# Performance work log

Measured on AMD Instinct MI355X. Metric: run time of the kernel, lower is better.

## Reference

```python
import jax, jax.numpy as jnp
import numpy as np

N_NODES = 100000
N_FEAT = 256
N_EDGES = 3200000
N_CLUSTERS = 16
COLLAPSE_REG = 0.1


def setup_inputs() -> dict:
    key = jax.random.key(0)
    k1, k2, k3, k4 = jax.random.split(key, 4)
    features = jax.random.normal(k1, (N_NODES, N_FEAT), dtype=jnp.float32)
    edge_row = jax.random.randint(k2, (N_EDGES,), 0, N_NODES, dtype=jnp.int32)
    edge_col = jax.random.randint(k3, (N_EDGES,), 0, N_NODES, dtype=jnp.int32)
    edge_val = jnp.ones((N_EDGES,), dtype=jnp.float32)
    # orthogonal-ish init approximated by scaled normal (init does not affect math)
    W = jax.random.normal(k4, (N_FEAT, N_CLUSTERS), dtype=jnp.float32) / np.float32(np.sqrt(N_FEAT))
    b = jnp.zeros((N_CLUSTERS,), dtype=jnp.float32)
    return {"features": features, "W": W, "b": b,
            "edge_row": edge_row, "edge_col": edge_col, "edge_val": edge_val}


def reference(features, W, b, edge_row, edge_col, edge_val):
    n = features.shape[0]
    k = W.shape[1]
    # assignment softmax (dropout_rate=0 -> identity)
    assignments = jax.nn.softmax(features @ W + b, axis=1)  # [n, k]
    cluster_sizes = assignments.sum(axis=0)                  # [k]
    assignments_pooling = assignments / cluster_sizes        # [n, k]
    # degrees = sparse row sums of adjacency
    degrees = jax.ops.segment_sum(edge_val, edge_row, num_segments=n)[:, None]  # [n, 1]
    n_edges = degrees.sum() / 2
    # sparse mm: adjacency @ assignments via gather + segment_sum
    adj_assign = jax.ops.segment_sum(edge_val[:, None] * assignments[edge_col],
                                     edge_row, num_segments=n)  # [n, k]
    graph_pooled = assignments.T @ adj_assign                # [k, k]
    normalizer_left = assignments.T @ degrees                # [k, 1]
    normalizer_right = degrees.T @ assignments               # [1, k]
    normalizer = normalizer_left @ normalizer_right / (2 * n_edges)
    spectral_loss = -jnp.trace(graph_pooled - normalizer) / (2 * n_edges)
    collapse_loss = COLLAPSE_REG * (jnp.linalg.norm(cluster_sizes) / n
                                    * jnp.sqrt(jnp.float32(k)) - 1.0)
    features_pooled = jax.nn.selu(assignments_pooling.T @ features)  # [k, d]
    return features_pooled, assignments, spectral_loss, collapse_loss
```

## Files before the change

### kernel.cpp

```cpp
#include <hip/hip_runtime.h>
#include <math.h>

#define KC 16
#define DF 256

#define WS_POOLED 0
#define WS_CS     4096
#define WS_M      4112
#define WS_TR     4128
#define WS_ESUM   4129
#define WS_TOTAL  4130
#define SHDW_OFF_BYTES 16640


typedef float floatx2 __attribute__((ext_vector_type(2)));

__global__ void zero_ws_kernel(float* __restrict__ ws) {
  int i = blockIdx.x * blockDim.x + threadIdx.x;
  if (i < WS_TOTAL) ws[i] = 0.0f;
}

__device__ __forceinline__ void cvt16_fp8(uint4 u, float* f) {
  floatx2 p;
  p = __builtin_amdgcn_cvt_pk_f32_fp8(u.x, false); f[0] = p[0];  f[1] = p[1];
  p = __builtin_amdgcn_cvt_pk_f32_fp8(u.x, true);  f[2] = p[0];  f[3] = p[1];
  p = __builtin_amdgcn_cvt_pk_f32_fp8(u.y, false); f[4] = p[0];  f[5] = p[1];
  p = __builtin_amdgcn_cvt_pk_f32_fp8(u.y, true);  f[6] = p[0];  f[7] = p[1];
  p = __builtin_amdgcn_cvt_pk_f32_fp8(u.z, false); f[8] = p[0];  f[9] = p[1];
  p = __builtin_amdgcn_cvt_pk_f32_fp8(u.z, true);  f[10] = p[0]; f[11] = p[1];
  p = __builtin_amdgcn_cvt_pk_f32_fp8(u.w, false); f[12] = p[0]; f[13] = p[1];
  p = __builtin_amdgcn_cvt_pk_f32_fp8(u.w, true);  f[14] = p[0]; f[15] = p[1];
}

__global__ void __launch_bounds__(256) assign_kernel(
    const float* __restrict__ F, const float* __restrict__ W,
    const float* __restrict__ b, float* __restrict__ S,
    unsigned* __restrict__ Sh, float* __restrict__ ws, int n) {
  __shared__ float Ft[32 * 257];
  __shared__ float cs_l[KC];
  const int t = threadIdx.x;
  if (t < KC) cs_l[t] = 0.0f;
  const int nb = blockIdx.x << 8;
  const int node = nb + t;
  const bool valid = node < n;
  const bool interior = (nb + 256 <= n);

  const int nl = t >> 3;
  const int jc = t & 7;

  float4 pref[8];
  auto load_chunk = [&](int s) {
    #pragma unroll
    for (int it = 0; it < 8; ++it) {
      const int nn = nl + (it << 5);
      if (interior || nb + nn < n)
        pref[it] = *(const float4*)&F[(size_t)(nb + nn) * DF + (s << 5) + (jc << 2)];
      else
        pref[it] = make_float4(0.f, 0.f, 0.f, 0.f);
    }
  };

  float acc[KC];
  #pragma unroll
  for (int k = 0; k < KC; ++k) acc[k] = 0.f;

  load_chunk(0);
  for (int s = 0; s < 8; ++s) {
    __syncthreads();
    #pragma unroll
    for (int it = 0; it < 8; ++it) {
      const int nn = nl + (it << 5);
      const int d0 = jc << 2;
      Ft[(d0 + 0) * 257 + nn] = pref[it].x;
      Ft[(d0 + 1) * 257 + nn] = pref[it].y;
      Ft[(d0 + 2) * 257 + nn] = pref[it].z;
      Ft[(d0 + 3) * 257 + nn] = pref[it].w;
    }
    __syncthreads();
    if (s < 7) load_chunk(s + 1);
    #pragma unroll
    for (int j = 0; j < 8; ++j) {
      const float fv0 = Ft[(4 * j + 0) * 257 + t];
      const float fv1 = Ft[(4 * j + 1) * 257 + t];
      const float fv2 = Ft[(4 * j + 2) * 257 + t];
      const float fv3 = Ft[(4 * j + 3) * 257 + t];
      const float* __restrict__ Wg = &W[(size_t)((s << 5) + (j << 2)) * KC];
      #pragma unroll
      for (int k = 0; k < KC; ++k)
        acc[k] += fv0 * Wg[k] + fv1 * Wg[KC + k]
                + fv2 * Wg[2 * KC + k] + fv3 * Wg[3 * KC + k];
    }
  }

  float mx = -1e30f;
  #pragma unroll
  for (int k = 0; k < KC; ++k) { acc[k] += b[k]; mx = fmaxf(mx, acc[k]); }
  float sum = 0.f;
  #pragma unroll
  for (int k = 0; k < KC; ++k) { acc[k] = __expf(acc[k] - mx); sum += acc[k]; }
  const float inv = 1.0f / sum;
  #pragma unroll
  for (int k = 0; k < KC; ++k) acc[k] *= inv;
  if (!valid) {
    #pragma unroll
    for (int k = 0; k < KC; ++k) acc[k] = 0.f;
  }
  if (valid) {
    float4* __restrict__ So = (float4*)&S[(size_t)node * KC];
    So[0] = make_float4(acc[0],  acc[1],  acc[2],  acc[3]);
    So[1] = make_float4(acc[4],  acc[5],  acc[6],  acc[7]);
    So[2] = make_float4(acc[8],  acc[9],  acc[10], acc[11]);
    So[3] = make_float4(acc[12], acc[13], acc[14], acc[15]);
    if (Sh) {
      unsigned w0, w1, w2, w3;
      w0 = __builtin_amdgcn_cvt_pk_fp8_f32(acc[0],  acc[1],  0,  false);
      w0 = __builtin_amdgcn_cvt_pk_fp8_f32(acc[2],  acc[3],  w0, true);
      w1 = __builtin_amdgcn_cvt_pk_fp8_f32(acc[4],  acc[5],  0,  false);
      w1 = __builtin_amdgcn_cvt_pk_fp8_f32(acc[6],  acc[7],  w1, true);
      w2 = __builtin_amdgcn_cvt_pk_fp8_f32(acc[8],  acc[9],  0,  false);
      w2 = __builtin_amdgcn_cvt_pk_fp8_f32(acc[10], acc[11], w2, true);
      w3 = __builtin_amdgcn_cvt_pk_fp8_f32(acc[12], acc[13], 0,  false);
      w3 = __builtin_amdgcn_cvt_pk_fp8_f32(acc[14], acc[15], w3, true);
      *(uint4*)&Sh[(size_t)node * 4] = make_uint4(w0, w1, w2, w3);
    }
  }
  #pragma unroll
  for (int off = 1; off < 64; off <<= 1) {
    #pragma unroll
    for (int k = 0; k < KC; ++k) acc[k] += __shfl_xor(acc[k], off);
  }
  if ((t & 63) == 0) {
    #pragma unroll
    for (int k = 0; k < KC; ++k) atomicAdd(&cs_l[k], acc[k]);
  }
  __syncthreads();
  if (t < KC) atomicAdd(&ws[WS_CS + t], cs_l[t]);
}

__global__ void __launch_bounds__(256) edge_kernel_fp8(
    const int* __restrict__ erow, const int* __restrict__ ecol,
    const float* __restrict__ evl, const uint4* __restrict__ S8,
    float* __restrict__ ws, int ne) {
  __shared__ float red[KC + 2];
  const int t = threadIdx.x;
  if (t < KC + 2) red[t] = 0.0f;
  __syncthreads();

  float m[KC];
  #pragma unroll
  for (int i = 0; i < KC; ++i) m[i] = 0.f;
  float tr = 0.f, es = 0.f;

  const int tid = blockIdx.x * 256 + t;
  const int stride = gridDim.x * 256;
  for (int e0 = tid; e0 < ne; e0 += 8 * stride) {
    int r[8], c[8];
    float v[8];
    #pragma unroll
    for (int q = 0; q < 8; ++q) {
      const int e = e0 + q * stride;
      const bool ok = (q == 0) || (e < ne);
      r[q] = ok ? erow[e] : 0;
      c[q] = ok ? ecol[e] : 0;
      v[q] = ok ? evl[e] : 0.f;
    }
    uint4 A[8], B[8];
    #pragma unroll
    for (int q = 0; q < 8; ++q) { A[q] = S8[r[q]]; B[q] = S8[c[q]]; }
    #pragma unroll
    for (int q = 0; q < 8; ++q) {
      float a[16], bb[16];
      cvt16_fp8(A[q], a);
      cvt16_fp8(B[q], bb);
      float d = 0.f;
      #pragma unroll
      for (int k = 0; k < 16; ++k) d += a[k] * bb[k];
      tr += v[q] * d;
      es += v[q];
      #pragma unroll
      for (int k = 0; k < 16; ++k) m[k] += v[q] * a[k];
    }
  }
  #pragma unroll
  for (int off = 1; off < 64; off <<= 1) {
    tr += __shfl_xor(tr, off);
    es += __shfl_xor(es, off);
    #pragma unroll
    for (int i = 0; i < KC; ++i) m[i] += __shfl_xor(m[i], off);
  }
  if ((t & 63) == 0) {
    atomicAdd(&red[KC], tr);
    atomicAdd(&red[KC + 1], es);
    #pragma unroll
    for (int i = 0; i < KC; ++i) atomicAdd(&red[i], m[i]);
  }
  __syncthreads();
  if (t < KC)            atomicAdd(&ws[WS_M + t], red[t]);
  else if (t == KC)      atomicAdd(&ws[WS_TR], red[KC]);
  else if (t == KC + 1)  atomicAdd(&ws[WS_ESUM], red[KC + 1]);
}

__global__ void __launch_bounds__(256) edge_kernel_f32(
    const int* __restrict__ erow, const int* __restrict__ ecol,
    const float* __restrict__ evl, const float* __restrict__ S,
    float* __restrict__ ws, int ne) {
  __shared__ float red[KC + 2];
  const int t = threadIdx.x;
  if (t < KC + 2) red[t] = 0.0f;
  __syncthreads();
  float m[KC];
  #pragma unroll
  for (int i = 0; i < KC; ++i) m[i] = 0.f;
  float tr = 0.f, es = 0.f;
  const int stride = gridDim.x * blockDim.x;
  for (int e = blockIdx.x * blockDim.x + t; e < ne; e += stride) {
    const int r = erow[e];
    const int c = ecol[e];
    const float v = evl[e];
    const float4* __restrict__ Sr = (const float4*)(S + (size_t)r * KC);
    const float4* __restrict__ Sc = (const float4*)(S + (size_t)c * KC);
    const float4 a0 = Sr[0], a1 = Sr[1], a2 = Sr[2], a3 = Sr[3];
    const float4 b0 = Sc[0], b1 = Sc[1], b2 = Sc[2], b3 = Sc[3];
    float d = a0.x*b0.x + a0.y*b0.y + a0.z*b0.z + a0.w*b0.w
            + a1.x*b1.x + a1.y*b1.y + a1.z*b1.z + a1.w*b1.w
            + a2.x*b2.x + a2.y*b2.y + a2.z*b2.z + a2.w*b2.w
            + a3.x*b3.x + a3.y*b3.y + a3.z*b3.z + a3.w*b3.w;
    tr += v * d; es += v;
    m[0]+=v*a0.x; m[1]+=v*a0.y; m[2]+=v*a0.z; m[3]+=v*a0.w;
    m[4]+=v*a1.x; m[5]+=v*a1.y; m[6]+=v*a1.z; m[7]+=v*a1.w;
    m[8]+=v*a2.x; m[9]+=v*a2.y; m[10]+=v*a2.z; m[11]+=v*a2.w;
    m[12]+=v*a3.x; m[13]+=v*a3.y; m[14]+=v*a3.z; m[15]+=v*a3.w;
  }
  #pragma unroll
  for (int off = 1; off < 64; off <<= 1) {
    tr += __shfl_xor(tr, off);
    es += __shfl_xor(es, off);
    #pragma unroll
    for (int i = 0; i < KC; ++i) m[i] += __shfl_xor(m[i], off);
  }
  if ((t & 63) == 0) {
    atomicAdd(&red[KC], tr);
    atomicAdd(&red[KC + 1], es);
    #pragma unroll
    for (int i = 0; i < KC; ++i) atomicAdd(&red[i], m[i]);
  }
  __syncthreads();
  if (t < KC)            atomicAdd(&ws[WS_M + t], red[t]);
  else if (t == KC)      atomicAdd(&ws[WS_TR], red[KC]);
  else if (t == KC + 1)  atomicAdd(&ws[WS_ESUM], red[KC + 1]);
}

__global__ void __launch_bounds__(256) pool_kernel(
    const float* __restrict__ F, const float* __restrict__ S,
    float* __restrict__ ws, int n) {
  const int t = threadIdx.x;
  float acc[KC];
  #pragma unroll
  for (int i = 0; i < KC; ++i) acc[i] = 0.f;

  const int nch = n >> 5;
  for (int ch = blockIdx.x; ch < nch; ch += gridDim.x) {
    const int base = ch << 5;
    float fl[32];
    #pragma unroll
    for (int i = 0; i < 32; ++i)
      fl[i] = F[(size_t)(base + i) * DF + t];
    #pragma unroll
    for (int i = 0; i < 32; ++i) {
      const float4* __restrict__ Sr = (const float4*)(S + (size_t)(base + i) * KC);
      const float4 s0 = Sr[0], s1 = Sr[1], s2 = Sr[2], s3 = Sr[3];
      const float f = fl[i];
      acc[0]+=f*s0.x;  acc[1]+=f*s0.y;  acc[2]+=f*s0.z;  acc[3]+=f*s0.w;
      acc[4]+=f*s1.x;  acc[5]+=f*s1.y;  acc[6]+=f*s1.z;  acc[7]+=f*s1.w;
      acc[8]+=f*s2.x;  acc[9]+=f*s2.y;  acc[10]+=f*s2.z; acc[11]+=f*s2.w;
      acc[12]+=f*s3.x; acc[13]+=f*s3.y; acc[14]+=f*s3.z; acc[15]+=f*s3.w;
    }
  }
  if (blockIdx.x == 0) {
    for (int i2 = nch << 5; i2 < n; ++i2) {
      const float f = F[(size_t)i2 * DF + t];
      const float* __restrict__ Sr = S + (size_t)i2 * KC;
      #pragma unroll
      for (int kk = 0; kk < KC; ++kk) acc[kk] += f * Sr[kk];
    }
  }
  #pragma unroll
  for (int kk = 0; kk < KC; ++kk)
    atomicAdd(&ws[WS_POOLED + kk * DF + t], acc[kk]);
}

__global__ void finalize_kernel(const float* __restrict__ ws,
                                float* __restrict__ out, int n) {
  const int t = threadIdx.x;
  const float alpha = 1.6732632423543772f;
  const float scale = 1.0507009873554805f;
  for (int idx = t; idx < KC * DF; idx += blockDim.x) {
    const int k = idx >> 8;
    const float x = ws[WS_POOLED + idx] / ws[WS_CS + k];
    const float r = x > 0.f ? x : alpha * expm1f(x);
    out[idx] = scale * r;
  }
  if (t == 0) {
    const float esum = ws[WS_ESUM];
    const float tr = ws[WS_TR];
    float sm2 = 0.f, sc2 = 0.f;
    for (int i = 0; i < KC; ++i) {
      const float mi = ws[WS_M + i];
      sm2 += mi * mi;
      const float ci = ws[WS_CS + i];
      sc2 += ci * ci;
    }
    const float spectral = -(tr - sm2 / esum) / esum;
    const float collapse = 0.1f * (sqrtf(sc2) / (float)n * 4.0f - 1.0f);
    const size_t off = (size_t)(KC * DF) + (size_t)n * KC;
    out[off] = spectral;
    out[off + 1] = collapse;
  }
}

extern "C" void kernel_launch(void* const* d_in, const int* in_sizes, int n_in,
                              void* d_out, int out_size, void* d_ws, size_t ws_size,
                              hipStream_t stream) {
  const float* F   = (const float*)d_in[0];
  const float* W   = (const float*)d_in[1];
  const float* b   = (const float*)d_in[2];
  const int* erow  = (const int*)d_in[3];
  const int* ecol  = (const int*)d_in[4];
  const float* evl = (const float*)d_in[5];
  const int n  = in_sizes[0] / DF;
  const int ne = in_sizes[3];
  float* out = (float*)d_out;
  float* S   = out + KC * DF;
  float* ws  = (float*)d_ws;

  const size_t shadow_bytes = (size_t)n * 16;
  const bool use_shadow = ws_size >= (size_t)SHDW_OFF_BYTES + shadow_bytes + 64;
  unsigned* Sh = use_shadow ? (unsigned*)((char*)d_ws + SHDW_OFF_BYTES) : nullptr;

  zero_ws_kernel<<<(WS_TOTAL + 255) / 256, 256, 0, stream>>>(ws);
  assign_kernel<<<(n + 255) / 256, 256, 0, stream>>>(F, W, b, S, Sh, ws, n);
  if (use_shadow)
    edge_kernel_fp8<<<1024, 256, 0, stream>>>(erow, ecol, evl, (const uint4*)Sh, ws, ne);
  else
    edge_kernel_f32<<<2048, 256, 0, stream>>>(erow, ecol, evl, S, ws, ne);
  pool_kernel<<<1024, 256, 0, stream>>>(F, S, ws, n);
  finalize_kernel<<<1, 256, 0, stream>>>(ws, out, n);
}
```

Before: 320.7 us.

## Double-buffer assign LDS tile, rotate pool atomics, retune edge and finalize grids

The assign kernel now alternates between two LDS transpose buffers, which drops one barrier per chunk, and asks for two blocks per CU through launch bounds. The pool kernel rotates the order of its atomic adds by block index so blocks spread across addresses instead of hitting the same ones together. The fp8 edge kernel grid grows from 1024 to 1792 blocks, and finalize is spread across 16 blocks instead of one. The larger LDS footprint and the launch-bounds register cap could reduce occupancy or cause spills.

```diff
diff --git a/kernel.cpp b/kernel.cpp
--- a/kernel.cpp
+++ b/kernel.cpp
@@ -32,11 +32,11 @@
   p = __builtin_amdgcn_cvt_pk_f32_fp8(u.w, true);  f[14] = p[0]; f[15] = p[1];
 }
 
-__global__ void __launch_bounds__(256) assign_kernel(
+__global__ void __launch_bounds__(256, 2) assign_kernel(
     const float* __restrict__ F, const float* __restrict__ W,
     const float* __restrict__ b, float* __restrict__ S,
     unsigned* __restrict__ Sh, float* __restrict__ ws, int n) {
-  __shared__ float Ft[32 * 257];
+  __shared__ float Ft[2][32 * 257];
   __shared__ float cs_l[KC];
   const int t = threadIdx.x;
   if (t < KC) cs_l[t] = 0.0f;
@@ -66,24 +66,24 @@
 
   load_chunk(0);
   for (int s = 0; s < 8; ++s) {
-    __syncthreads();
+    float* __restrict__ B = Ft[s & 1];
     #pragma unroll
     for (int it = 0; it < 8; ++it) {
       const int nn = nl + (it << 5);
       const int d0 = jc << 2;
-      Ft[(d0 + 0) * 257 + nn] = pref[it].x;
-      Ft[(d0 + 1) * 257 + nn] = pref[it].y;
-      Ft[(d0 + 2) * 257 + nn] = pref[it].z;
-      Ft[(d0 + 3) * 257 + nn] = pref[it].w;
+      B[(d0 + 0) * 257 + nn] = pref[it].x;
+      B[(d0 + 1) * 257 + nn] = pref[it].y;
+      B[(d0 + 2) * 257 + nn] = pref[it].z;
+      B[(d0 + 3) * 257 + nn] = pref[it].w;
     }
     __syncthreads();
     if (s < 7) load_chunk(s + 1);
     #pragma unroll
     for (int j = 0; j < 8; ++j) {
-      const float fv0 = Ft[(4 * j + 0) * 257 + t];
-      const float fv1 = Ft[(4 * j + 1) * 257 + t];
-      const float fv2 = Ft[(4 * j + 2) * 257 + t];
-      const float fv3 = Ft[(4 * j + 3) * 257 + t];
+      const float fv0 = B[(4 * j + 0) * 257 + t];
+      const float fv1 = B[(4 * j + 1) * 257 + t];
+      const float fv2 = B[(4 * j + 2) * 257 + t];
+      const float fv3 = B[(4 * j + 3) * 257 + t];
       const float* __restrict__ Wg = &W[(size_t)((s << 5) + (j << 2)) * KC];
       #pragma unroll
       for (int k = 0; k < KC; ++k)
@@ -284,23 +284,26 @@
       for (int kk = 0; kk < KC; ++kk) acc[kk] += f * Sr[kk];
     }
   }
-  #pragma unroll
-  for (int kk = 0; kk < KC; ++kk)
-    atomicAdd(&ws[WS_POOLED + kk * DF + t], acc[kk]);
+  const int rot = blockIdx.x & 15;
+  #pragma unroll
+  for (int kk = 0; kk < KC; ++kk) {
+    const int kidx = (kk + rot) & 15;
+    atomicAdd(&ws[WS_POOLED + kidx * DF + t], acc[kidx]);
+  }
 }
 
 __global__ void finalize_kernel(const float* __restrict__ ws,
                                 float* __restrict__ out, int n) {
-  const int t = threadIdx.x;
+  const int idx = blockIdx.x * 256 + threadIdx.x;
   const float alpha = 1.6732632423543772f;
   const float scale = 1.0507009873554805f;
-  for (int idx = t; idx < KC * DF; idx += blockDim.x) {
+  if (idx < KC * DF) {
     const int k = idx >> 8;
     const float x = ws[WS_POOLED + idx] / ws[WS_CS + k];
     const float r = x > 0.f ? x : alpha * expm1f(x);
     out[idx] = scale * r;
   }
-  if (t == 0) {
+  if (idx == 0) {
     const float esum = ws[WS_ESUM];
     const float tr = ws[WS_TR];
     float sm2 = 0.f, sc2 = 0.f;
@@ -340,9 +343,9 @@
   zero_ws_kernel<<<(WS_TOTAL + 255) / 256, 256, 0, stream>>>(ws);
   assign_kernel<<<(n + 255) / 256, 256, 0, stream>>>(F, W, b, S, Sh, ws, n);
   if (use_shadow)
-    edge_kernel_fp8<<<1024, 256, 0, stream>>>(erow, ecol, evl, (const uint4*)Sh, ws, ne);
+    edge_kernel_fp8<<<1792, 256, 0, stream>>>(erow, ecol, evl, (const uint4*)Sh, ws, ne);
   else
     edge_kernel_f32<<<2048, 256, 0, stream>>>(erow, ecol, evl, S, ws, ne);
   pool_kernel<<<1024, 256, 0, stream>>>(F, S, ws, n);
-  finalize_kernel<<<1, 256, 0, stream>>>(ws, out, n);
-}
+  finalize_kernel<<<16, 256, 0, stream>>>(ws, out, n);
+}
```

Measured after the change: 320.9 us. No clear change (+0.1%).
